# Performance work log

Measured on AMD Instinct MI355X. Metric: run time of the kernel, lower is better.

## Reference

```python
import jax, jax.numpy as jnp
import numpy as np

B, L, D = 4, 8192, 512


def setup_inputs() -> dict:
    key = jax.random.key(0)
    kx, kwg, kwc = jax.random.split(key, 3)
    x = jax.random.normal(kx, (B, L, D), dtype=jnp.float32)
    # Xavier-uniform init for DxD linears
    bound = float(np.sqrt(6.0 / (D + D)))
    Wg = jax.random.uniform(kwg, (D, D), minval=-bound, maxval=bound, dtype=jnp.float32)
    bg = jnp.ones((D,), dtype=jnp.float32)   # gate bias init to 1.0
    Wc = jax.random.uniform(kwc, (D, D), minval=-bound, maxval=bound, dtype=jnp.float32)
    bc = jnp.zeros((D,), dtype=jnp.float32)
    return {"x": x, "Wg": Wg, "bg": bg, "Wc": Wc, "bc": bc}


def _mingru_scan(gates, cands):
    # h_t = (1 - g_t) * h_{t-1} + g_t * c_t, h_0 = 0
    # linear recurrence h_t = a_t h_{t-1} + b_t with a = 1-g, b = g*c
    a = 1.0 - gates
    b = gates * cands

    def combine(left, right):
        a_l, b_l = left
        a_r, b_r = right
        return a_r * a_l, a_r * b_l + b_r

    _, h = jax.lax.associative_scan(combine, (a, b), axis=1)
    return h


def reference(x, Wg, bg, Wc, bc):
    gates = jax.nn.sigmoid(jnp.einsum('bld,ed->ble', x, Wg) + bg)
    cands = jnp.tanh(jnp.einsum('bld,ed->ble', x, Wc) + bc)
    return _mingru_scan(gates, cands)
```

## Files before the change

kernel.cpp:

```cpp
#include <hip/hip_runtime.h>
#include <stdint.h>
#include <stddef.h>

#define B_ 4
#define L_ 8192
#define D_ 512
#define M_ (B_*L_)
#define K_ 512
#define CHUNK 64
#define NC (L_/CHUNK)

typedef _Float16 f16;
typedef f16 f16x2 __attribute__((ext_vector_type(2)));
typedef f16 f16x4 __attribute__((ext_vector_type(4)));
typedef f16 f16x8 __attribute__((ext_vector_type(8)));
typedef float f32x4 __attribute__((ext_vector_type(4)));

__device__ __forceinline__ void async16(const void* g, void* l) {
  __builtin_amdgcn_global_load_lds(
      (const __attribute__((address_space(1))) uint32_t*)g,
      (__attribute__((address_space(3))) uint32_t*)l,
      16, 0, 0);
}

__global__ __launch_bounds__(256) void prep(const float* __restrict__ x,
                                            const float* __restrict__ Wg,
                                            const float* __restrict__ Wc,
                                            f16* __restrict__ xh,
                                            f16* __restrict__ wp) {
  const int bid = blockIdx.x;
  if (bid < 16384) {
    const int idx = (bid * 256 + threadIdx.x) * 4;
    float4 v = *(const float4*)(x + idx);
    f16x4 o = {(f16)v.x, (f16)v.y, (f16)v.z, (f16)v.w};
    *(f16x4*)(xh + idx) = o;
  } else {
    const int idx = ((bid - 16384) * 256 + threadIdx.x) * 4;
    const float* src = (idx < 262144) ? (Wg + idx) : (Wc + (idx - 262144));
    float4 v = *(const float4*)src;
    f16x4 o = {(f16)v.x, (f16)v.y, (f16)v.z, (f16)v.w};
    *(f16x4*)(wp + idx) = o;
  }
}

__global__ __launch_bounds__(256, 2) void gemm_act(
    const f16* __restrict__ Xh, const f16* __restrict__ Wp,
    const float* __restrict__ bg, const float* __restrict__ bc,
    uint32_t* __restrict__ AC,
    float* __restrict__ cA, float* __restrict__ cB) {
  __shared__ __align__(16) f16 sA[2][128 * 32];
  __shared__ __align__(16) f16 sBg[2][128 * 32];
  __shared__ __align__(16) f16 sBc[2][128 * 32];

  const int tid = threadIdx.x;
  const int id = blockIdx.x;
  const int xcd = id & 7;
  const int slot = id >> 3;
  const int g_ = xcd * 128 + slot;
  const int bm = g_ >> 2;
  const int bn = g_ & 3;

  const int lane = tid & 63;
  const int w = tid >> 6;
  const int wm = w >> 1, wn = w & 1;
  const int l15 = lane & 15, quad = lane >> 4;

  const int srow = tid >> 2;
  const int spc8 = (tid & 3) * 8;
  const f16* gA  = Xh + (size_t)(bm * 128 + srow) * K_ + spc8;
  const f16* gBg = Wp + (size_t)(bn * 128 + srow) * K_ + spc8;
  const f16* gBc = Wp + (size_t)(512 + bn * 128 + srow) * K_ + spc8;

  f32x4 accG[4][4] = {};
  f32x4 accC[4][4] = {};

#define STAGE(kk, b) { \
    async16(gA + (kk),  &sA[b][tid * 8]); \
    async16(gA + (size_t)64 * K_ + (kk),  &sA[b][tid * 8 + 64 * 32]); \
    async16(gBg + (kk), &sBg[b][tid * 8]); \
    async16(gBg + (size_t)64 * K_ + (kk), &sBg[b][tid * 8 + 64 * 32]); \
    async16(gBc + (kk), &sBc[b][tid * 8]); \
    async16(gBc + (size_t)64 * K_ + (kk), &sBc[b][tid * 8 + 64 * 32]); }

#define COMPUTE(bC) { \
    f16x8 af[4], bgf[4], bcf[4]; \
    _Pragma("unroll") \
    for (int i = 0; i < 4; i++) \
      af[i] = *(const f16x8*)(&sA[bC][(wm * 64 + i * 16 + l15) * 32 + quad * 8]); \
    _Pragma("unroll") \
    for (int j = 0; j < 4; j++) { \
      bgf[j] = *(const f16x8*)(&sBg[bC][(wn * 64 + j * 16 + l15) * 32 + quad * 8]); \
      bcf[j] = *(const f16x8*)(&sBc[bC][(wn * 64 + j * 16 + l15) * 32 + quad * 8]); \
    } \
    _Pragma("unroll") \
    for (int i = 0; i < 4; i++) \
      _Pragma("unroll") \
      for (int j = 0; j < 4; j++) { \
        accG[i][j] = __builtin_amdgcn_mfma_f32_16x16x32_f16(af[i], bgf[j], accG[i][j], 0, 0, 0); \
        accC[i][j] = __builtin_amdgcn_mfma_f32_16x16x32_f16(af[i], bcf[j], accC[i][j], 0, 0, 0); \
      } }

  STAGE(0, 0);
  asm volatile("s_waitcnt vmcnt(0)" ::: "memory");
  __builtin_amdgcn_s_barrier();

#pragma unroll
  for (int t = 0; t < 15; t++) {
    const int c = t & 1, n = c ^ 1;
    STAGE((t + 1) * 32, n);
    COMPUTE(c);
    asm volatile("s_waitcnt vmcnt(0)" ::: "memory");
    __builtin_amdgcn_s_barrier();
  }
  COMPUTE(1);
#undef COMPUTE
#undef STAGE

  const int c = bm * 2 + wm;
#pragma unroll
  for (int j = 0; j < 4; j++) {
    const int col = bn * 128 + wn * 64 + j * 16 + l15;
    const float bgv = bg[col];
    const float bcv = bc[col];
    float blkP[4], blkQ[4];
#pragma unroll
    for (int i = 0; i < 4; i++) {
      const int mrow = bm * 128 + wm * 64 + i * 16 + quad * 4;
      float P = 1.0f, Q = 0.0f;
#pragma unroll
      for (int r = 0; r < 4; r++) {
        float yg = accG[i][j][r] + bgv;
        float gg = 1.0f / (1.0f + __expf(-yg));
        float yc = accC[i][j][r] + bcv;
        yc = fminf(fmaxf(yc, -15.0f), 15.0f);
        float t = __expf(2.0f * yc);
        float cc = (t - 1.0f) / (t + 1.0f);
        f16x2 p;
        p[0] = (f16)(1.0f - gg);
        p[1] = (f16)(gg * cc);
        *(f16x2*)&AC[(size_t)(mrow + r) * 512 + col] = p;
        const float av = (float)p[0];
        const float bv = (float)p[1];
        Q = fmaf(av, Q, bv);
        P *= av;
      }
      float Pp = __shfl_xor(P, 16);
      float Qp = __shfl_xor(Q, 16);
      float nP = P * Pp;
      float nQ = (quad & 1) ? fmaf(P, Qp, Q) : fmaf(Pp, Q, Qp);
      Pp = __shfl_xor(nP, 32);
      Qp = __shfl_xor(nQ, 32);
      blkP[i] = nP * Pp;
      blkQ[i] = (quad & 2) ? fmaf(nP, Qp, nQ) : fmaf(Pp, nQ, Qp);
    }
    float CP = blkP[0], CQ = blkQ[0];
#pragma unroll
    for (int i = 1; i < 4; i++) {
      CQ = fmaf(blkP[i], CQ, blkQ[i]);
      CP *= blkP[i];
    }
    if (quad == 0) {
      cA[(size_t)c * 512 + col] = CP;
      cB[(size_t)c * 512 + col] = CQ;
    }
  }
}

__global__ __launch_bounds__(256) void scan_apply(
    const uint32_t* __restrict__ AC,
    const float* __restrict__ cA, const float* __restrict__ cB,
    float* __restrict__ out) {
  const int blk = blockIdx.x;
  const int ch = blk & (NC - 1);
  const int bseq = blk >> 7;
  const int d0 = threadIdx.x * 2;

  float h0 = 0.0f, h1 = 0.0f;
  const float* pA = cA + (size_t)(bseq * NC) * 512 + d0;
  const float* pB = cB + (size_t)(bseq * NC) * 512 + d0;
#pragma unroll 4
  for (int cc = 0; cc < ch; cc++) {
    float2 va = *(const float2*)(pA + (size_t)cc * 512);
    float2 vb = *(const float2*)(pB + (size_t)cc * 512);
    h0 = fmaf(va.x, h0, vb.x);
    h1 = fmaf(va.y, h1, vb.y);
  }

  const size_t base = (size_t)blk * CHUNK * 512 + d0;
#pragma unroll 8
  for (int t = 0; t < CHUNK; t++) {
    const size_t i = base + (size_t)t * 512;
    uint2 v = *(const uint2*)&AC[i];
    f16x2 p0 = __builtin_bit_cast(f16x2, v.x);
    f16x2 p1 = __builtin_bit_cast(f16x2, v.y);
    h0 = fmaf((float)p0[0], h0, (float)p0[1]);
    h1 = fmaf((float)p1[0], h1, (float)p1[1]);
    float2 o;
    o.x = h0;
    o.y = h1;
    *(float2*)&out[i] = o;
  }
}

extern "C" void kernel_launch(void* const* d_in, const int* in_sizes, int n_in,
                              void* d_out, int out_size, void* d_ws, size_t ws_size,
                              hipStream_t stream) {
  const float* x  = (const float*)d_in[0];
  const float* Wg = (const float*)d_in[1];
  const float* bg = (const float*)d_in[2];
  const float* Wc = (const float*)d_in[3];
  const float* bc = (const float*)d_in[4];
  float* out = (float*)d_out;

  char* ws = (char*)d_ws;
  f16*      xh = (f16*)(ws);
  f16*      wp = (f16*)(ws + 33554432);
  uint32_t* AC = (uint32_t*)(ws + 34603008);
  float*    cA = (float*)(ws + 101711872);
  float*    cB = (float*)(ws + 102760448);

  prep<<<16896, 256, 0, stream>>>(x, Wg, Wc, xh, wp);
  gemm_act<<<(M_ / 128) * 4, 256, 0, stream>>>(xh, wp, bg, bc, AC, cA, cB);
  scan_apply<<<B_ * NC, 256, 0, stream>>>(AC, cA, cB, out);
}
```

Before: 206.8 us.

## Add separate chunk-prefix scan kernel and widen prep conversion to 8 elements

A small scan_chunks kernel now computes the exclusive prefix state for each chunk once, in serial over 128 chunks per (batch, channel), and stores it to a new workspace buffer. scan_apply loads that prefix directly instead of having every block redo an O(chunk index) loop over cA/cB, which removes quadratic redundant reads and evens out the per-block work. The prep kernel now converts 8 floats per thread with half as many blocks. The trade-off is an extra launch plus a 32-block serial kernel with low parallelism and a 128-step dependency chain.

```diff
diff --git a/kernel.cpp b/kernel.cpp
--- a/kernel.cpp
+++ b/kernel.cpp
@@ -12,7 +12,6 @@
 
 typedef _Float16 f16;
 typedef f16 f16x2 __attribute__((ext_vector_type(2)));
-typedef f16 f16x4 __attribute__((ext_vector_type(4)));
 typedef f16 f16x8 __attribute__((ext_vector_type(8)));
 typedef float f32x4 __attribute__((ext_vector_type(4)));
 
@@ -29,18 +28,18 @@
                                             f16* __restrict__ xh,
                                             f16* __restrict__ wp) {
   const int bid = blockIdx.x;
-  if (bid < 16384) {
-    const int idx = (bid * 256 + threadIdx.x) * 4;
-    float4 v = *(const float4*)(x + idx);
-    f16x4 o = {(f16)v.x, (f16)v.y, (f16)v.z, (f16)v.w};
-    *(f16x4*)(xh + idx) = o;
-  } else {
-    const int idx = ((bid - 16384) * 256 + threadIdx.x) * 4;
-    const float* src = (idx < 262144) ? (Wg + idx) : (Wc + (idx - 262144));
-    float4 v = *(const float4*)src;
-    f16x4 o = {(f16)v.x, (f16)v.y, (f16)v.z, (f16)v.w};
-    *(f16x4*)(wp + idx) = o;
-  }
+  const int isX = (bid < 8192);
+  const int U = (isX ? bid : (bid - 8192)) * 256 + threadIdx.x;
+  const float* src;
+  f16* dst;
+  if (isX)            { src = x + (size_t)U * 8;                     dst = xh; }
+  else if (U < 32768) { src = Wg + (size_t)U * 8;                    dst = wp; }
+  else                { src = Wc + (size_t)(U - 32768) * 8;          dst = wp; }
+  float4 v0 = *(const float4*)src;
+  float4 v1 = *(const float4*)(src + 4);
+  f16x8 o = {(f16)v0.x, (f16)v0.y, (f16)v0.z, (f16)v0.w,
+             (f16)v1.x, (f16)v1.y, (f16)v1.z, (f16)v1.w};
+  *(f16x8*)(dst + (size_t)U * 8) = o;
 }
 
 __global__ __launch_bounds__(256, 2) void gemm_act(
@@ -166,39 +165,36 @@
   }
 }
 
+__global__ __launch_bounds__(64) void scan_chunks(
+    const float* __restrict__ cA, const float* __restrict__ cB,
+    float* __restrict__ Hpre) {
+  const int b = blockIdx.x >> 3;
+  const int d = ((blockIdx.x & 7) << 6) + threadIdx.x;
+  float h = 0.0f;
+#pragma unroll 8
+  for (int ch = 0; ch < NC; ch++) {
+    const int idx = (b * NC + ch) * 512 + d;
+    Hpre[idx] = h;
+    h = fmaf(cA[idx], h, cB[idx]);
+  }
+}
+
 __global__ __launch_bounds__(256) void scan_apply(
-    const uint32_t* __restrict__ AC,
-    const float* __restrict__ cA, const float* __restrict__ cB,
+    const uint32_t* __restrict__ AC, const float* __restrict__ Hpre,
     float* __restrict__ out) {
   const int blk = blockIdx.x;
-  const int ch = blk & (NC - 1);
-  const int bseq = blk >> 7;
   const int d0 = threadIdx.x * 2;
-
-  float h0 = 0.0f, h1 = 0.0f;
-  const float* pA = cA + (size_t)(bseq * NC) * 512 + d0;
-  const float* pB = cB + (size_t)(bseq * NC) * 512 + d0;
-#pragma unroll 4
-  for (int cc = 0; cc < ch; cc++) {
-    float2 va = *(const float2*)(pA + (size_t)cc * 512);
-    float2 vb = *(const float2*)(pB + (size_t)cc * 512);
-    h0 = fmaf(va.x, h0, vb.x);
-    h1 = fmaf(va.y, h1, vb.y);
-  }
-
+  float2 h = *(const float2*)&Hpre[blk * 512 + d0];
   const size_t base = (size_t)blk * CHUNK * 512 + d0;
-#pragma unroll 8
+#pragma unroll 16
   for (int t = 0; t < CHUNK; t++) {
     const size_t i = base + (size_t)t * 512;
     uint2 v = *(const uint2*)&AC[i];
     f16x2 p0 = __builtin_bit_cast(f16x2, v.x);
     f16x2 p1 = __builtin_bit_cast(f16x2, v.y);
-    h0 = fmaf((float)p0[0], h0, (float)p0[1]);
-    h1 = fmaf((float)p1[0], h1, (float)p1[1]);
-    float2 o;
-    o.x = h0;
-    o.y = h1;
-    *(float2*)&out[i] = o;
+    h.x = fmaf((float)p0[0], h.x, (float)p0[1]);
+    h.y = fmaf((float)p1[0], h.y, (float)p1[1]);
+    *(float2*)&out[i] = h;
   }
 }
 
@@ -218,8 +214,10 @@
   uint32_t* AC = (uint32_t*)(ws + 34603008);
   float*    cA = (float*)(ws + 101711872);
   float*    cB = (float*)(ws + 102760448);
-
-  prep<<<16896, 256, 0, stream>>>(x, Wg, Wc, xh, wp);
+  float*    Hp = (float*)(ws + 103809024);
+
+  prep<<<8448, 256, 0, stream>>>(x, Wg, Wc, xh, wp);
   gemm_act<<<(M_ / 128) * 4, 256, 0, stream>>>(xh, wp, bg, bc, AC, cA, cB);
-  scan_apply<<<B_ * NC, 256, 0, stream>>>(AC, cA, cB, out);
-}
+  scan_chunks<<<32, 64, 0, stream>>>(cA, cB, Hp);
+  scan_apply<<<B_ * NC, 256, 0, stream>>>(AC, Hp, out);
+}
```

Result: slower. 211.2 us (+2.1%).
